# Performance work log

Hardware: AMD Instinct MI355X
Metric: run time of the kernel (lower is better)

## Reference

```python
import jax, jax.numpy as jnp
import numpy as np

GROUP = 64

def dequant(W_q, scale, zero):
    # W_q: [out, in] int, scale/zero: [out, in//GROUP]
    out, din = W_q.shape
    g = din // GROUP
    Wq = W_q.reshape(out, g, GROUP).astype(scale.dtype)
    W = (Wq - zero[:, :, None]) * scale[:, :, None]
    return W.reshape(out, din)

def setup_inputs() -> dict:
    key = jax.random.key(0)
    ks = jax.random.split(key, 10)
    T, H, F = 512, 4096, 14336
    return {
        "hidden_states": jax.random.normal(ks[0], (T, H), jnp.float32),
        "W1_q": jax.random.randint(ks[1], (F, H), 0, 16, jnp.int32),
        "w1_scale": jax.random.uniform(ks[2], (F, H // GROUP), jnp.float32, 1e-3, 0.02),
        "w1_zero": jax.random.uniform(ks[3], (F, H // GROUP), jnp.float32, 6.0, 9.0),
        "W3_q": jax.random.randint(ks[4], (F, H), 0, 16, jnp.int32),
        "w3_scale": jax.random.uniform(ks[5], (F, H // GROUP), jnp.float32, 1e-3, 0.02),
        "w3_zero": jax.random.uniform(ks[6], (F, H // GROUP), jnp.float32, 6.0, 9.0),
        "W2_q": jax.random.randint(ks[7], (H, F), 0, 16, jnp.int32),
        "w2_scale": jax.random.uniform(ks[8], (H, F // GROUP), jnp.float32, 1e-3, 0.02),
        "w2_zero": jax.random.uniform(ks[9], (H, F // GROUP), jnp.float32, 6.0, 9.0),
    }

def reference(hidden_states, W1_q, w1_scale, w1_zero, W3_q, w3_scale, w3_zero, W2_q, w2_scale, w2_zero):
    W1 = dequant(W1_q, w1_scale, w1_zero)  # [F, H]
    W3 = dequant(W3_q, w3_scale, w3_zero)  # [F, H]
    W2 = dequant(W2_q, w2_scale, w2_zero)  # [H, F]
    g = jax.nn.silu(hidden_states @ W1.T) * (hidden_states @ W3.T)  # [T, F]
    return g @ W2.T  # [T, H]
```

## Files before the change

### kernel.cpp

```cpp
#include <hip/hip_runtime.h>
#include <hip/hip_bf16.h>

#define T_DIM 512
#define H_DIM 4096
#define F_DIM 14336
#define KSEG  8

typedef __attribute__((ext_vector_type(8))) short bf16x8;
typedef __attribute__((ext_vector_type(4))) float f32x4;

__device__ __forceinline__ unsigned short f2bf(float f) {
    union { __hip_bfloat16 h; unsigned short u; } cv;
    cv.h = __float2bfloat16(f);
    return cv.u;
}

__device__ __forceinline__ void dq16(int4 qv, float s, float z, unsigned short* dst) {
    float nzs = -z * s;
    ushort4 o;
    o.x = f2bf(fmaf((float)qv.x, s, nzs));
    o.y = f2bf(fmaf((float)qv.y, s, nzs));
    o.z = f2bf(fmaf((float)qv.z, s, nzs));
    o.w = f2bf(fmaf((float)qv.w, s, nzs));
    *(ushort4*)dst = o;
}

__global__ __launch_bounds__(256) void zero_out(float4* __restrict__ out) {
    out[blockIdx.x * 256 + threadIdx.x] = make_float4(0.f, 0.f, 0.f, 0.f);
}

__global__ __launch_bounds__(256) void cvt_x(const float* __restrict__ X,
                                             unsigned short* __restrict__ Xb) {
    int i = (blockIdx.x * 256 + threadIdx.x) * 4;
    float4 v = *(const float4*)&X[i];
    ushort4 o;
    o.x = f2bf(v.x); o.y = f2bf(v.y); o.z = f2bf(v.z); o.w = f2bf(v.w);
    *(ushort4*)&Xb[i] = o;
}

__global__ __launch_bounds__(256, 2)
void gate_up_kernel(const unsigned short* __restrict__ Xb,
                    const int* __restrict__ W1q, const float* __restrict__ sc1,
                    const float* __restrict__ zp1,
                    const int* __restrict__ W3q, const float* __restrict__ sc3,
                    const float* __restrict__ zp3,
                    unsigned short* __restrict__ G)
{
    constexpr int LK = 72;
    constexpr int BUFB = (128 + 64 + 64) * LK * 2;
    __shared__ __align__(16) char smem[2 * BUFB];
    float* sEx = (float*)smem;

    const int t = threadIdx.x, wave = t >> 6, lane = t & 63;
    const int r = lane & 15, q = lane >> 4;
    const int mh  = (wave & 1) * 64;
    const int mat = wave >> 1;

    const int b = blockIdx.x;
    const int xcd = b & 7, lb = b >> 3;
    const int m0 = (lb & 3) * 128;
    const int n0 = (xcd * 28 + (lb >> 2)) * 64;
    const int SG = H_DIM / 64;

    const int xrow = t >> 3, xch = (t & 7) * 8;
    const int wrow = t >> 4, wc = (t & 15) * 4;

    int4 pW1[4], pW3[4];
    #pragma unroll
    for (int i = 0; i < 4; ++i) {
        size_t off = (size_t)(n0 + wrow + 16 * i) * H_DIM + wc;
        pW1[i] = *(const int4*)&W1q[off];
        pW3[i] = *(const int4*)&W3q[off];
    }

    {
        unsigned short* sX  = (unsigned short*)smem;
        unsigned short* sW1 = (unsigned short*)(smem + 128 * LK * 2);
        unsigned short* sW3 = (unsigned short*)(smem + 192 * LK * 2);
        #pragma unroll
        for (int i = 0; i < 4; ++i) {
            int4 xv = *(const int4*)&Xb[(size_t)(m0 + xrow + 32 * i) * H_DIM + xch];
            *(int4*)&sX[(xrow + 32 * i) * LK + xch] = xv;
        }
        #pragma unroll
        for (int i = 0; i < 4; ++i) {
            int row = wrow + 16 * i;
            int sidx = (n0 + row) * SG;
            dq16(pW1[i], sc1[sidx], zp1[sidx], &sW1[row * LK + wc]);
            dq16(pW3[i], sc3[sidx], zp3[sidx], &sW3[row * LK + wc]);
        }
        #pragma unroll
        for (int i = 0; i < 4; ++i) {
            size_t off = (size_t)(n0 + wrow + 16 * i) * H_DIM + 64 + wc;
            pW1[i] = *(const int4*)&W1q[off];
            pW3[i] = *(const int4*)&W3q[off];
        }
    }
    __syncthreads();

    f32x4 acc[4][4];
    #pragma unroll
    for (int a = 0; a < 4; ++a)
        #pragma unroll
        for (int c = 0; c < 4; ++c) acc[a][c] = (f32x4){0.f, 0.f, 0.f, 0.f};

    constexpr int NIT = H_DIM / 64;
    #pragma unroll 2
    for (int it = 0; it < NIT; ++it) {
        const char* cb = smem + (it & 1) * BUFB;
        const unsigned short* sX = (const unsigned short*)cb;
        const unsigned short* sB =
            (const unsigned short*)(cb + (mat ? 192 : 128) * LK * 2);

        #pragma unroll
        for (int kh = 0; kh < 2; ++kh) {
            const int kb = kh * 32 + q * 8;
            bf16x8 av[4], bv[4];
            #pragma unroll
            for (int im = 0; im < 4; ++im)
                av[im] = *(const bf16x8*)&sX[(mh + im * 16 + r) * LK + kb];
            #pragma unroll
            for (int j = 0; j < 4; ++j)
                bv[j] = *(const bf16x8*)&sB[(j * 16 + r) * LK + kb];
            #pragma unroll
            for (int im = 0; im < 4; ++im)
                #pragma unroll
                for (int j = 0; j < 4; ++j)
                    acc[im][j] = __builtin_amdgcn_mfma_f32_16x16x32_bf16(av[im], bv[j], acc[im][j], 0, 0, 0);
        }

        if (it < NIT - 1) {
            char* nb = smem + ((it + 1) & 1) * BUFB;
            unsigned short* nX  = (unsigned short*)nb;
            unsigned short* nW1 = (unsigned short*)(nb + 128 * LK * 2);
            unsigned short* nW3 = (unsigned short*)(nb + 192 * LK * 2);
            const int kn = (it + 1) * 64;
            #pragma unroll
            for (int i = 0; i < 4; ++i) {
                int4 xv = *(const int4*)&Xb[(size_t)(m0 + xrow + 32 * i) * H_DIM + kn + xch];
                *(int4*)&nX[(xrow + 32 * i) * LK + xch] = xv;
            }
            const int gidx = it + 1;
            #pragma unroll
            for (int i = 0; i < 4; ++i) {
                int row = wrow + 16 * i;
                int sidx = (n0 + row) * SG + gidx;
                dq16(pW1[i], sc1[sidx], zp1[sidx], &nW1[row * LK + wc]);
                dq16(pW3[i], sc3[sidx], zp3[sidx], &nW3[row * LK + wc]);
            }
            if (it < NIT - 2) {
                const int kf = (it + 2) * 64;
                #pragma unroll
                for (int i = 0; i < 4; ++i) {
                    size_t off = (size_t)(n0 + wrow + 16 * i) * H_DIM + kf + wc;
                    pW1[i] = *(const int4*)&W1q[off];
                    pW3[i] = *(const int4*)&W3q[off];
                }
            }
            __syncthreads();
        }
    }

    if (mat == 1) {
        #pragma unroll
        for (int im = 0; im < 4; ++im)
            #pragma unroll
            for (int j = 0; j < 4; ++j)
                #pragma unroll
                for (int reg = 0; reg < 4; ++reg)
                    sEx[(mh + im * 16 + q * 4 + reg) * 65 + j * 16 + r] = acc[im][j][reg];
    }
    __syncthreads();
    if (mat == 0) {
        #pragma unroll
        for (int im = 0; im < 4; ++im)
            #pragma unroll
            for (int j = 0; j < 4; ++j)
                #pragma unroll
                for (int reg = 0; reg < 4; ++reg) {
                    int ml = mh + im * 16 + q * 4 + reg;
                    int nl = j * 16 + r;
                    float g1 = acc[im][j][reg];
                    float g3 = sEx[ml * 65 + nl];
                    float val = g1 / (1.f + __expf(-g1)) * g3;
                    G[(size_t)(m0 + ml) * F_DIM + n0 + nl] = f2bf(val);
                }
    }
}

__global__ __launch_bounds__(256, 2)
void down_kernel(const unsigned short* __restrict__ G,
                 const int* __restrict__ W2q, const float* __restrict__ sc2,
                 const float* __restrict__ zp2,
                 float* __restrict__ Out)
{
    constexpr int LK = 72;
    constexpr int BUFB = (128 + 128) * LK * 2;
    __shared__ __align__(16) char smem[2 * BUFB];

    const int t = threadIdx.x, wave = t >> 6, lane = t & 63;
    const int r = lane & 15, q = lane >> 4;
    const int wm = (wave & 1) * 64, wn = (wave >> 1) * 64;

    const int b = blockIdx.x;
    const int xcd = b & 7, lb = b >> 3;
    const int m0 = (lb & 3) * 128;
    const int pair = xcd * 32 + (lb >> 2);
    const int n0 = (pair >> 3) * 128;
    const int kbeg = (pair & 7) * (F_DIM / KSEG);
    const int SG = F_DIM / 64;

    const int arow = t >> 3, ach = (t & 7) * 8;
    const int wrow = t >> 4, wc = (t & 15) * 4;

    int4 pW[8];
    #pragma unroll
    for (int i = 0; i < 8; ++i)
        pW[i] = *(const int4*)&W2q[(size_t)(n0 + wrow + 16 * i) * F_DIM + kbeg + wc];

    {
        unsigned short* sA = (unsigned short*)smem;
        unsigned short* sW = (unsigned short*)(smem + 128 * LK * 2);
        #pragma unroll
        for (int i = 0; i < 4; ++i) {
            int4 gv = *(const int4*)&G[(size_t)(m0 + arow + 32 * i) * F_DIM + kbeg + ach];
            *(int4*)&sA[(arow + 32 * i) * LK + ach] = gv;
        }
        const int gidx = kbeg >> 6;
        #pragma unroll
        for (int i = 0; i < 8; ++i) {
            int row = wrow + 16 * i;
            int sidx = (n0 + row) * SG + gidx;
            dq16(pW[i], sc2[sidx], zp2[sidx], &sW[row * LK + wc]);
        }
        #pragma unroll
        for (int i = 0; i < 8; ++i)
            pW[i] = *(const int4*)&W2q[(size_t)(n0 + wrow + 16 * i) * F_DIM + kbeg + 64 + wc];
    }
    __syncthreads();

    f32x4 acc[4][4];
    #pragma unroll
    for (int a = 0; a < 4; ++a)
        #pragma unroll
        for (int c = 0; c < 4; ++c) acc[a][c] = (f32x4){0.f, 0.f, 0.f, 0.f};

    constexpr int NIT = (F_DIM / KSEG) / 64;
    #pragma unroll 2
    for (int it = 0; it < NIT; ++it) {
        const char* cb = smem + (it & 1) * BUFB;
        const unsigned short* sA = (const unsigned short*)cb;
        const unsigned short* sW = (const unsigned short*)(cb + 128 * LK * 2);

        #pragma unroll
        for (int kh = 0; kh < 2; ++kh) {
            const int kb = kh * 32 + q * 8;
            bf16x8 av[4], bv[4];
            #pragma unroll
            for (int im = 0; im < 4; ++im)
                av[im] = *(const bf16x8*)&sA[(wm + im * 16 + r) * LK + kb];
            #pragma unroll
            for (int j = 0; j < 4; ++j)
                bv[j] = *(const bf16x8*)&sW[(wn + j * 16 + r) * LK + kb];
            #pragma unroll
            for (int im = 0; im < 4; ++im)
                #pragma unroll
                for (int j = 0; j < 4; ++j)
                    acc[im][j] = __builtin_amdgcn_mfma_f32_16x16x32_bf16(av[im], bv[j], acc[im][j], 0, 0, 0);
        }

        if (it < NIT - 1) {
            char* nb = smem + ((it + 1) & 1) * BUFB;
            unsigned short* nA = (unsigned short*)nb;
            unsigned short* nW = (unsigned short*)(nb + 128 * LK * 2);
            const int kn = kbeg + (it + 1) * 64;
            #pragma unroll
            for (int i = 0; i < 4; ++i) {
                int4 gv = *(const int4*)&G[(size_t)(m0 + arow + 32 * i) * F_DIM + kn + ach];
                *(int4*)&nA[(arow + 32 * i) * LK + ach] = gv;
            }
            const int gidx = kn >> 6;
            #pragma unroll
            for (int i = 0; i < 8; ++i) {
                int row = wrow + 16 * i;
                int sidx = (n0 + row) * SG + gidx;
                dq16(pW[i], sc2[sidx], zp2[sidx], &nW[row * LK + wc]);
            }
            if (it < NIT - 2) {
                const int kf = kbeg + (it + 2) * 64;
                #pragma unroll
                for (int i = 0; i < 8; ++i)
                    pW[i] = *(const int4*)&W2q[(size_t)(n0 + wrow + 16 * i) * F_DIM + kf + wc];
            }
            __syncthreads();
        }
    }

    #pragma unroll
    for (int im = 0; im < 4; ++im)
        #pragma unroll
        for (int j = 0; j < 4; ++j)
            #pragma unroll
            for (int reg = 0; reg < 4; ++reg) {
                int m = m0 + wm + im * 16 + q * 4 + reg;
                int h = n0 + wn + j * 16 + r;
                atomicAdd(&Out[(size_t)m * H_DIM + h], acc[im][j][reg]);
            }
}

extern "C" void kernel_launch(void* const* d_in, const int* in_sizes, int n_in,
                              void* d_out, int out_size, void* d_ws, size_t ws_size,
                              hipStream_t stream) {
    const float* X   = (const float*)d_in[0];
    const int*   W1q = (const int*)d_in[1];
    const float* s1  = (const float*)d_in[2];
    const float* z1  = (const float*)d_in[3];
    const int*   W3q = (const int*)d_in[4];
    const float* s3  = (const float*)d_in[5];
    const float* z3  = (const float*)d_in[6];
    const int*   W2q = (const int*)d_in[7];
    const float* s2  = (const float*)d_in[8];
    const float* z2  = (const float*)d_in[9];
    float* Out = (float*)d_out;

    unsigned short* Xb = (unsigned short*)d_ws;
    unsigned short* G  = (unsigned short*)((char*)d_ws + (4 << 20));

    zero_out<<<2048, 256, 0, stream>>>((float4*)Out);
    cvt_x<<<2048, 256, 0, stream>>>(X, Xb);
    gate_up_kernel<<<896, 256, 0, stream>>>(Xb, W1q, s1, z1, W3q, s3, z3, G);
    down_kernel<<<1024, 256, 0, stream>>>(G, W2q, s2, z2, Out);
}
```

Before: 873.3 us.

## Load activation tiles directly to LDS with XOR swizzle and shorten weight prefetch

Both GEMM kernels now move the bf16 activation tile (X or G) from global memory straight into LDS with global_load_lds, skipping registers. An XOR-swizzled unpadded layout replaces the old padding to avoid bank conflicts. The quantized weight prefetch is reduced from two iterations ahead to one, issued at the top of each iteration before the MFMAs. This lowers register pressure and VALU/LDS store work but gives less lead time to hide weight load latency, and it relies on the async LDS load finishing before the barrier.

```diff
diff --git a/kernel.cpp b/kernel.cpp
--- a/kernel.cpp
+++ b/kernel.cpp
@@ -23,6 +23,12 @@
     o.z = f2bf(fmaf((float)qv.z, s, nzs));
     o.w = f2bf(fmaf((float)qv.w, s, nzs));
     *(ushort4*)dst = o;
+}
+
+__device__ __forceinline__ void gload16(const void* g, void* l) {
+    __builtin_amdgcn_global_load_lds(
+        (const __attribute__((address_space(1))) void*)(unsigned long long)(uintptr_t)g,
+        (__attribute__((address_space(3))) void*)(uintptr_t)l, 16, 0, 0);
 }
 
 __global__ __launch_bounds__(256) void zero_out(float4* __restrict__ out) {
@@ -47,7 +53,9 @@
                     unsigned short* __restrict__ G)
 {
     constexpr int LK = 72;
-    constexpr int BUFB = (128 + 64 + 64) * LK * 2;
+    constexpr int XB = 128 * 64 * 2;
+    constexpr int WB = 64 * LK * 2;
+    constexpr int BUFB = XB + 2 * WB;
     __shared__ __align__(16) char smem[2 * BUFB];
     float* sEx = (float*)smem;
 
@@ -55,6 +63,7 @@
     const int r = lane & 15, q = lane >> 4;
     const int mh  = (wave & 1) * 64;
     const int mat = wave >> 1;
+    const int rs  = r & 7;
 
     const int b = blockIdx.x;
     const int xcd = b & 7, lb = b >> 3;
@@ -62,26 +71,27 @@
     const int n0 = (xcd * 28 + (lb >> 2)) * 64;
     const int SG = H_DIM / 64;
 
-    const int xrow = t >> 3, xch = (t & 7) * 8;
     const int wrow = t >> 4, wc = (t & 15) * 4;
 
+    const int lrow = lane >> 3;
+    const int lc   = (lane & 7) ^ lrow;
+    const unsigned short* xsrc =
+        Xb + (size_t)(m0 + wave * 32 + lrow) * H_DIM + lc * 8;
+
     int4 pW1[4], pW3[4];
-    #pragma unroll
-    for (int i = 0; i < 4; ++i) {
-        size_t off = (size_t)(n0 + wrow + 16 * i) * H_DIM + wc;
-        pW1[i] = *(const int4*)&W1q[off];
-        pW3[i] = *(const int4*)&W3q[off];
-    }
 
     {
-        unsigned short* sX  = (unsigned short*)smem;
-        unsigned short* sW1 = (unsigned short*)(smem + 128 * LK * 2);
-        unsigned short* sW3 = (unsigned short*)(smem + 192 * LK * 2);
         #pragma unroll
         for (int i = 0; i < 4; ++i) {
-            int4 xv = *(const int4*)&Xb[(size_t)(m0 + xrow + 32 * i) * H_DIM + xch];
-            *(int4*)&sX[(xrow + 32 * i) * LK + xch] = xv;
-        }
+            size_t off = (size_t)(n0 + wrow + 16 * i) * H_DIM + wc;
+            pW1[i] = *(const int4*)&W1q[off];
+            pW3[i] = *(const int4*)&W3q[off];
+        }
+        #pragma unroll
+        for (int j = 0; j < 4; ++j)
+            gload16(xsrc + (size_t)j * 8 * H_DIM, smem + (wave * 4 + j) * 1024);
+        unsigned short* sW1 = (unsigned short*)(smem + XB);
+        unsigned short* sW3 = (unsigned short*)(smem + XB + WB);
         #pragma unroll
         for (int i = 0; i < 4; ++i) {
             int row = wrow + 16 * i;
@@ -89,12 +99,6 @@
             dq16(pW1[i], sc1[sidx], zp1[sidx], &sW1[row * LK + wc]);
             dq16(pW3[i], sc3[sidx], zp3[sidx], &sW3[row * LK + wc]);
         }
-        #pragma unroll
-        for (int i = 0; i < 4; ++i) {
-            size_t off = (size_t)(n0 + wrow + 16 * i) * H_DIM + 64 + wc;
-            pW1[i] = *(const int4*)&W1q[off];
-            pW3[i] = *(const int4*)&W3q[off];
-        }
     }
     __syncthreads();
 
@@ -108,17 +112,32 @@
     #pragma unroll 2
     for (int it = 0; it < NIT; ++it) {
         const char* cb = smem + (it & 1) * BUFB;
+        char* nb = smem + ((it + 1) & 1) * BUFB;
+        const int kn = (it + 1) * 64;
+
+        if (it + 1 < NIT) {
+            #pragma unroll
+            for (int i = 0; i < 4; ++i) {
+                size_t off = (size_t)(n0 + wrow + 16 * i) * H_DIM + kn + wc;
+                pW1[i] = *(const int4*)&W1q[off];
+                pW3[i] = *(const int4*)&W3q[off];
+            }
+            #pragma unroll
+            for (int j = 0; j < 4; ++j)
+                gload16(xsrc + (size_t)j * 8 * H_DIM + kn,
+                        nb + (wave * 4 + j) * 1024);
+        }
+
         const unsigned short* sX = (const unsigned short*)cb;
-        const unsigned short* sB =
-            (const unsigned short*)(cb + (mat ? 192 : 128) * LK * 2);
-
+        const unsigned short* sB = (const unsigned short*)(cb + XB + mat * WB);
         #pragma unroll
         for (int kh = 0; kh < 2; ++kh) {
             const int kb = kh * 32 + q * 8;
+            const int xc = (kh * 4 + q) ^ rs;
             bf16x8 av[4], bv[4];
             #pragma unroll
             for (int im = 0; im < 4; ++im)
-                av[im] = *(const bf16x8*)&sX[(mh + im * 16 + r) * LK + kb];
+                av[im] = *(const bf16x8*)&sX[(mh + im * 16 + r) * 64 + xc * 8];
             #pragma unroll
             for (int j = 0; j < 4; ++j)
                 bv[j] = *(const bf16x8*)&sB[(j * 16 + r) * LK + kb];
@@ -129,17 +148,9 @@
                     acc[im][j] = __builtin_amdgcn_mfma_f32_16x16x32_bf16(av[im], bv[j], acc[im][j], 0, 0, 0);
         }
 
-        if (it < NIT - 1) {
-            char* nb = smem + ((it + 1) & 1) * BUFB;
-            unsigned short* nX  = (unsigned short*)nb;
-            unsigned short* nW1 = (unsigned short*)(nb + 128 * LK * 2);
-            unsigned short* nW3 = (unsigned short*)(nb + 192 * LK * 2);
-            const int kn = (it + 1) * 64;
-            #pragma unroll
-            for (int i = 0; i < 4; ++i) {
-                int4 xv = *(const int4*)&Xb[(size_t)(m0 + xrow + 32 * i) * H_DIM + kn + xch];
-                *(int4*)&nX[(xrow + 32 * i) * LK + xch] = xv;
-            }
+        if (it + 1 < NIT) {
+            unsigned short* nW1 = (unsigned short*)(nb + XB);
+            unsigned short* nW3 = (unsigned short*)(nb + XB + WB);
             const int gidx = it + 1;
             #pragma unroll
             for (int i = 0; i < 4; ++i) {
@@ -147,15 +158,6 @@
                 int sidx = (n0 + row) * SG + gidx;
                 dq16(pW1[i], sc1[sidx], zp1[sidx], &nW1[row * LK + wc]);
                 dq16(pW3[i], sc3[sidx], zp3[sidx], &nW3[row * LK + wc]);
-            }
-            if (it < NIT - 2) {
-                const int kf = (it + 2) * 64;
-                #pragma unroll
-                for (int i = 0; i < 4; ++i) {
-                    size_t off = (size_t)(n0 + wrow + 16 * i) * H_DIM + kf + wc;
-                    pW1[i] = *(const int4*)&W1q[off];
-                    pW3[i] = *(const int4*)&W3q[off];
-                }
             }
             __syncthreads();
         }
@@ -195,12 +197,15 @@
                  float* __restrict__ Out)
 {
     constexpr int LK = 72;
-    constexpr int BUFB = (128 + 128) * LK * 2;
+    constexpr int AB = 128 * 64 * 2;
+    constexpr int WB = 128 * LK * 2;
+    constexpr int BUFB = AB + WB;
     __shared__ __align__(16) char smem[2 * BUFB];
 
     const int t = threadIdx.x, wave = t >> 6, lane = t & 63;
     const int r = lane & 15, q = lane >> 4;
     const int wm = (wave & 1) * 64, wn = (wave >> 1) * 64;
+    const int rs = r & 7;
 
     const int b = blockIdx.x;
     const int xcd = b & 7, lb = b >> 3;
@@ -210,22 +215,23 @@
     const int kbeg = (pair & 7) * (F_DIM / KSEG);
     const int SG = F_DIM / 64;
 
-    const int arow = t >> 3, ach = (t & 7) * 8;
     const int wrow = t >> 4, wc = (t & 15) * 4;
 
+    const int lrow = lane >> 3;
+    const int lc   = (lane & 7) ^ lrow;
+    const unsigned short* asrc =
+        G + (size_t)(m0 + wave * 32 + lrow) * F_DIM + kbeg + lc * 8;
+
     int4 pW[8];
-    #pragma unroll
-    for (int i = 0; i < 8; ++i)
-        pW[i] = *(const int4*)&W2q[(size_t)(n0 + wrow + 16 * i) * F_DIM + kbeg + wc];
 
     {
-        unsigned short* sA = (unsigned short*)smem;
-        unsigned short* sW = (unsigned short*)(smem + 128 * LK * 2);
-        #pragma unroll
-        for (int i = 0; i < 4; ++i) {
-            int4 gv = *(const int4*)&G[(size_t)(m0 + arow + 32 * i) * F_DIM + kbeg + ach];
-            *(int4*)&sA[(arow + 32 * i) * LK + ach] = gv;
-        }
+        #pragma unroll
+        for (int i = 0; i < 8; ++i)
+            pW[i] = *(const int4*)&W2q[(size_t)(n0 + wrow + 16 * i) * F_DIM + kbeg + wc];
+        #pragma unroll
+        for (int j = 0; j < 4; ++j)
+            gload16(asrc + (size_t)j * 8 * F_DIM, smem + (wave * 4 + j) * 1024);
+        unsigned short* sW = (unsigned short*)(smem + AB);
         const int gidx = kbeg >> 6;
         #pragma unroll
         for (int i = 0; i < 8; ++i) {
@@ -233,9 +239,6 @@
             int sidx = (n0 + row) * SG + gidx;
             dq16(pW[i], sc2[sidx], zp2[sidx], &sW[row * LK + wc]);
         }
-        #pragma unroll
-        for (int i = 0; i < 8; ++i)
-            pW[i] = *(const int4*)&W2q[(size_t)(n0 + wrow + 16 * i) * F_DIM + kbeg + 64 + wc];
     }
     __syncthreads();
 
@@ -249,16 +252,29 @@
     #pragma unroll 2
     for (int it = 0; it < NIT; ++it) {
         const char* cb = smem + (it & 1) * BUFB;
+        char* nb = smem + ((it + 1) & 1) * BUFB;
+        const int kn = kbeg + (it + 1) * 64;
+
+        if (it + 1 < NIT) {
+            #pragma unroll
+            for (int i = 0; i < 8; ++i)
+                pW[i] = *(const int4*)&W2q[(size_t)(n0 + wrow + 16 * i) * F_DIM + kn + wc];
+            #pragma unroll
+            for (int j = 0; j < 4; ++j)
+                gload16(asrc + (size_t)j * 8 * F_DIM + (it + 1) * 64,
+                        nb + (wave * 4 + j) * 1024);
+        }
+
         const unsigned short* sA = (const unsigned short*)cb;
-        const unsigned short* sW = (const unsigned short*)(cb + 128 * LK * 2);
-
+        const unsigned short* sW = (const unsigned short*)(cb + AB);
         #pragma unroll
         for (int kh = 0; kh < 2; ++kh) {
             const int kb = kh * 32 + q * 8;
+            const int xc = (kh * 4 + q) ^ rs;
             bf16x8 av[4], bv[4];
             #pragma unroll
             for (int im = 0; im < 4; ++im)
-                av[im] = *(const bf16x8*)&sA[(wm + im * 16 + r) * LK + kb];
+                av[im] = *(const bf16x8*)&sA[(wm + im * 16 + r) * 64 + xc * 8];
             #pragma unroll
             for (int j = 0; j < 4; ++j)
                 bv[j] = *(const bf16x8*)&sW[(wn + j * 16 + r) * LK + kb];
@@ -269,28 +285,14 @@
                     acc[im][j] = __builtin_amdgcn_mfma_f32_16x16x32_bf16(av[im], bv[j], acc[im][j], 0, 0, 0);
         }
 
-        if (it < NIT - 1) {
-            char* nb = smem + ((it + 1) & 1) * BUFB;
-            unsigned short* nA = (unsigned short*)nb;
-            unsigned short* nW = (unsigned short*)(nb + 128 * LK * 2);
-            const int kn = kbeg + (it + 1) * 64;
-            #pragma unroll
-            for (int i = 0; i < 4; ++i) {
-                int4 gv = *(const int4*)&G[(size_t)(m0 + arow + 32 * i) * F_DIM + kn + ach];
-                *(int4*)&nA[(arow + 32 * i) * LK + ach] = gv;
-            }
+        if (it + 1 < NIT) {
+            unsigned short* nW = (unsigned short*)(nb + AB);
             const int gidx = kn >> 6;
             #pragma unroll
             for (int i = 0; i < 8; ++i) {
                 int row = wrow + 16 * i;
                 int sidx = (n0 + row) * SG + gidx;
                 dq16(pW[i], sc2[sidx], zp2[sidx], &nW[row * LK + wc]);
-            }
-            if (it < NIT - 2) {
-                const int kf = kbeg + (it + 2) * 64;
-                #pragma unroll
-                for (int i = 0; i < 8; ++i)
-                    pW[i] = *(const int4*)&W2q[(size_t)(n0 + wrow + 16 * i) * F_DIM + kf + wc];
             }
             __syncthreads();
         }
```

After: 940.1 us. 7.7% more time.
